# Optimization experiments

Hardware: AMD Instinct MI355X
Metric: run time of the kernel (lower is better)

Reference implementation:

```python
import jax, jax.numpy as jnp
import numpy as np

B, CQ, CM, K, O = 8, 128, 128, 128, 128
LQ, LK = 2048, 2048


def setup_inputs() -> dict:
    key = jax.random.key(0)
    ks = jax.random.split(key, 8)
    s = 0.05
    return {
        "x1": jax.random.normal(ks[0], (B, CQ, LQ), dtype=jnp.float32),
        "x2": jax.random.normal(ks[1], (B, CM, LK), dtype=jnp.float32),
        "Wq": jax.random.normal(ks[2], (K, CQ), dtype=jnp.float32) * s,
        "bq": jax.random.normal(ks[3], (K,), dtype=jnp.float32) * s,
        "Wk": jax.random.normal(ks[4], (K, CM), dtype=jnp.float32) * s,
        "bk": jax.random.normal(ks[5], (K,), dtype=jnp.float32) * s,
        "Wv": jax.random.normal(ks[6], (O, CM), dtype=jnp.float32) * s,
        "bv": jax.random.normal(ks[7], (O,), dtype=jnp.float32) * s,
    }


def reference(x1, x2, Wq, bq, Wk, bk, Wv, bv):
    # Conv1d with kernel_size=1 == per-position linear over channels
    q = jnp.einsum("bcq,kc->bkq", x1, Wq) + bq[None, :, None]  # (B,K,Lq)
    k = jnp.einsum("bcm,kc->bkm", x2, Wk) + bk[None, :, None]  # (B,K,Lk)
    v = jnp.einsum("bcm,oc->bom", x2, Wv) + bv[None, :, None]  # (B,O,Lk)
    # u[b,m,q] = sum_k q[b,k,q]*k[b,k,m] / sqrt(K)   -> (B,Lk,Lq)
    scale = 1.0 / np.sqrt(q.shape[1]).astype(np.float32)
    u = jnp.einsum("bkq,bkm->bmq", q, k) * scale
    w = jax.nn.softmax(u, axis=1)  # softmax over Lk (torch dim=1)
    # out[b,o,q] = sum_m w[b,m,q]*v[b,o,m]   -> (B,O,Lq)
    out = jnp.einsum("bmq,bom->boq", w, v)
    return (out, w)
```

## Files before the change

kernel.cpp:

```cpp
#include <hip/hip_runtime.h>
#include <cstddef>

#define B_ 8
#define C_ 128
#define K_ 128
#define L_ 2048

static constexpr float SCALE = 0.08838834764831843f;

typedef unsigned short u16;
typedef __attribute__((ext_vector_type(8))) short bf16x8;
typedef __attribute__((ext_vector_type(4))) unsigned short u16x4;
typedef __attribute__((ext_vector_type(4))) unsigned int u32x4;
typedef __attribute__((ext_vector_type(4))) float f32x4;
typedef __attribute__((ext_vector_type(16))) float f32x16;

__device__ __forceinline__ u16 f2bf(float x) {
    unsigned u = __builtin_bit_cast(unsigned, x);
    u += 0x7FFFu + ((u >> 16) & 1u);
    return (u16)(u >> 16);
}

__device__ __forceinline__ unsigned cvtpk(float lo, float hi) {
    unsigned r;
    asm("v_cvt_pk_bf16_f32 %0, %1, %2" : "=v"(r) : "v"(lo), "v"(hi));
    return r;
}
__device__ __forceinline__ void plswap(unsigned& a, unsigned& b) {
    asm volatile("v_permlane32_swap_b32 %0, %1" : "+v"(a), "+v"(b));
}

#define MFMA32 __builtin_amdgcn_mfma_f32_32x32x16_bf16


__global__ __launch_bounds__(256) void xpose_kernel(
    const float* __restrict__ x1, const float* __restrict__ x2,
    u16* __restrict__ xT1, u16* __restrict__ xT2)
{
    const int src = blockIdx.z;
    const int b   = blockIdx.y;
    const int l   = blockIdx.x * 128 + (threadIdx.x & 127);
    const int half = threadIdx.x >> 7;
    const float* X = src ? x2 : x1;
    u16* dst       = src ? xT2 : xT1;
    const float* xb = X + ((size_t)b * C_ + half * 64) * L_ + l;
    u16* db = dst + ((size_t)b * L_ + l) * C_ + half * 64;
    for (int c0 = 0; c0 < 64; c0 += 8) {
        bf16x8 pk;
        #pragma unroll
        for (int j = 0; j < 8; ++j)
            pk[j] = (short)f2bf(xb[(size_t)(c0 + j) * L_]);
        *(bf16x8*)(db + c0) = pk;
    }
}

__global__ __launch_bounds__(256) void proj_kernel(
    const u16* __restrict__ xT1, const u16* __restrict__ xT2,
    const float* __restrict__ Wq, const float* __restrict__ bq,
    const float* __restrict__ Wk, const float* __restrict__ bk,
    const float* __restrict__ Wv, const float* __restrict__ bv,
    u16* __restrict__ qF, u16* __restrict__ kF, u16* __restrict__ vF)
{
    const int l0 = blockIdx.x * 64;
    const int p  = blockIdx.y % 3;
    const int b  = blockIdx.y / 3;
    const float* W    = (p == 0) ? Wq : (p == 1) ? Wk : Wv;
    const float* bias = (p == 0) ? bq : (p == 1) ? bk : bv;
    const u16* xT     = (p == 0) ? xT1 : xT2;

    __shared__ u16 Wls[128 * 136];
    const int tid = threadIdx.x;
    for (int i = tid; i < 4096; i += 256) {
        float4 v = ((const float4*)W)[i];
        int e = i << 2; int row = e >> 7; int colc = e & 127;
        u16x4 pk = { f2bf(v.x), f2bf(v.y), f2bf(v.z), f2bf(v.w) };
        *(u16x4*)&Wls[row * 136 + colc] = pk;
    }
    __syncthreads();

    const int w = tid >> 6, l = tid & 63;
    const int lr = l & 15, lg = l >> 4;
    const int lrow = l0 + w * 16 + lr;

    bf16x8 xfr[4];
    const u16* xb = xT + ((size_t)b * L_ + lrow) * C_;
    #pragma unroll
    for (int s = 0; s < 4; ++s)
        xfr[s] = *(const bf16x8*)(xb + s * 32 + lg * 8);

    const int hl2 = lg >> 1, j0 = (lg & 1) * 4;

    for (int kt = 0; kt < 8; ++kt) {
        bf16x8 wfr[4];
        #pragma unroll
        for (int s = 0; s < 4; ++s)
            wfr[s] = *(const bf16x8*)&Wls[(kt * 16 + lr) * 136 + s * 32 + lg * 8];
        f32x4 acc = {0.f, 0.f, 0.f, 0.f};
        if (p < 2) {
            #pragma unroll
            for (int s = 0; s < 4; ++s)
                acc = __builtin_amdgcn_mfma_f32_16x16x32_bf16(wfr[s], xfr[s], acc, 0, 0, 0);
            u16x4 pk;
            #pragma unroll
            for (int r = 0; r < 4; ++r)
                pk[r] = f2bf(acc[r] + bias[kt * 16 + lg * 4 + r]);
            const int qt = lrow >> 5, qloc = lrow & 31;
            u16* dstp = ((p == 0) ? qF : kF)
                + (((size_t)b * 64 + qt) * 8 + kt) * 512 + hl2 * 256 + qloc * 8 + j0;
            *(u16x4*)dstp = pk;
        } else {
            #pragma unroll
            for (int s = 0; s < 4; ++s)
                acc = __builtin_amdgcn_mfma_f32_16x16x32_bf16(xfr[s], wfr[s], acc, 0, 0, 0);
            const int o = kt * 16 + lr;
            const float bo = bias[o];
            u16x4 pk;
            #pragma unroll
            for (int r = 0; r < 4; ++r)
                pk[r] = f2bf(acc[r] + bo);
            const int mt  = (l0 >> 5) + ((w * 16 + lg * 4) >> 5);
            const int t   = w & 1;
            const int ob  = kt >> 1;
            const int oloc = (kt & 1) * 16 + lr;
            u16* dstp = vF + ((size_t)b * 64 + mt) * 4096
                + ob * 1024 + t * 512 + hl2 * 256 + oloc * 8 + j0;
            *(u16x4*)dstp = pk;
        }
    }
}

__global__ __launch_bounds__(256, 2) void fused_attn_kernel(
    const u16* __restrict__ qF, const u16* __restrict__ kF,
    const u16* __restrict__ vF, float* __restrict__ out,
    float* __restrict__ wout)
{
    __shared__ float red[4 * 128 * 32];

    const int bid = blockIdx.x;
    const int b   = bid & 7;
    const int qt  = bid >> 3;
    const int q0  = qt * 32;
    const int tid = threadIdx.x;
    const int w   = tid >> 6;
    const int l   = tid & 63;
    const int col = l & 31;
    const int hl  = l >> 5;
    const int mz  = w * 512;

    bf16x8 qf[8];
    {
        const u16* qp = qF + (((size_t)b * 64 + qt) * 8) * 512 + l * 8;
        #pragma unroll
        for (int ks = 0; ks < 8; ++ks)
            qf[ks] = *(const bf16x8*)(qp + ks * 512);
    }

    const u16* kbase = kF + (((size_t)b * 64 + (mz >> 5)) * 8) * 512 + l * 8;
    const u16* vbase = vF + ((size_t)b * 64 + (mz >> 5)) * 4096 + l * 8;

    bf16x8 kA[8], kB[8];
    auto LK = [&](bf16x8 (&d)[8], int it) {
        const u16* ka = kbase + (size_t)it * 4096;
        #pragma unroll
        for (int j = 0; j < 8; ++j)
            d[j] = *(const bf16x8*)(ka + j * 512);
    };

    float csum = 0.f;
    auto STEPA = [&](bf16x8 (&kf)[8], bf16x8 (&kn)[8], int itn) {
        f32x16 sa = {}, sb = {};
        sa = MFMA32(kf[0], qf[0], sa, 0, 0, 0); sb = MFMA32(kf[4], qf[4], sb, 0, 0, 0);
        sa = MFMA32(kf[1], qf[1], sa, 0, 0, 0); sb = MFMA32(kf[5], qf[5], sb, 0, 0, 0);
        sa = MFMA32(kf[2], qf[2], sa, 0, 0, 0); sb = MFMA32(kf[6], qf[6], sb, 0, 0, 0);
        sa = MFMA32(kf[3], qf[3], sa, 0, 0, 0); sb = MFMA32(kf[7], qf[7], sb, 0, 0, 0);
        LK(kn, itn);
        float e[16];
        #pragma unroll
        for (int r = 0; r < 16; ++r)
            e[r] = __expf((sa[r] + sb[r]) * SCALE);
        float c0 = (e[0] + e[1]) + (e[2] + e[3]);
        float c1 = (e[4] + e[5]) + (e[6] + e[7]);
        float c2 = (e[8] + e[9]) + (e[10] + e[11]);
        float c3 = (e[12] + e[13]) + (e[14] + e[15]);
        csum += (c0 + c1) + (c2 + c3);
    };

    LK(kA, 0);
    for (int i2 = 0; i2 < 8; ++i2) {
        STEPA(kA, kB, 2 * i2 + 1);
        STEPA(kB, kA, (2 * i2 + 2) & 15);
    }

    csum += __shfl_xor(csum, 32);
    if (hl == 0) red[w * 32 + col] = csum;
    __syncthreads();
    const float rs = 1.0f / (red[col] + red[32 + col] + red[64 + col] + red[96 + col]);
    __syncthreads();

    f32x16 pv0 = {}, pv1 = {}, pv2 = {}, pv3 = {};

    auto STEPB = [&](bf16x8 (&kf)[8], int it, bf16x8 (&kn)[8]) {
        const u16* va = vbase + (size_t)it * 4096;
        bf16x8 vf[8];
        #pragma unroll
        for (int j = 0; j < 8; ++j)
            vf[j] = *(const bf16x8*)(va + j * 512);

        f32x16 sa = {}, sb = {};
        sa = MFMA32(kf[0], qf[0], sa, 0, 0, 0); sb = MFMA32(kf[4], qf[4], sb, 0, 0, 0);
        sa = MFMA32(kf[1], qf[1], sa, 0, 0, 0); sb = MFMA32(kf[5], qf[5], sb, 0, 0, 0);
        sa = MFMA32(kf[2], qf[2], sa, 0, 0, 0); sb = MFMA32(kf[6], qf[6], sb, 0, 0, 0);
        sa = MFMA32(kf[3], qf[3], sa, 0, 0, 0); sb = MFMA32(kf[7], qf[7], sb, 0, 0, 0);

        LK(kn, (it + 1) & 15);

        float e[16];
        #pragma unroll
        for (int r = 0; r < 16; ++r)
            e[r] = __expf((sa[r] + sb[r]) * SCALE);

        unsigned R0 = cvtpk(e[0], e[1]),   R1 = cvtpk(e[2], e[3]);
        unsigned R2 = cvtpk(e[4], e[5]),   R3 = cvtpk(e[6], e[7]);
        unsigned R4 = cvtpk(e[8], e[9]),   R5 = cvtpk(e[10], e[11]);
        unsigned R6 = cvtpk(e[12], e[13]), R7 = cvtpk(e[14], e[15]);
        plswap(R0, R2); plswap(R1, R3); plswap(R4, R6); plswap(R5, R7);
        u32x4 w0v = { R0, R1, R2, R3 };
        u32x4 w1v = { R4, R5, R6, R7 };
        bf16x8 B0 = __builtin_bit_cast(bf16x8, w0v);
        bf16x8 B1 = __builtin_bit_cast(bf16x8, w1v);

        pv0 = MFMA32(vf[0], B0, pv0, 0, 0, 0); pv1 = MFMA32(vf[2], B0, pv1, 0, 0, 0);
        pv2 = MFMA32(vf[4], B0, pv2, 0, 0, 0); pv3 = MFMA32(vf[6], B0, pv3, 0, 0, 0);
        pv0 = MFMA32(vf[1], B1, pv0, 0, 0, 0); pv1 = MFMA32(vf[3], B1, pv1, 0, 0, 0);
        pv2 = MFMA32(vf[5], B1, pv2, 0, 0, 0); pv3 = MFMA32(vf[7], B1, pv3, 0, 0, 0);

        float* wp = wout + ((size_t)b * L_ + mz + it * 32) * L_ + q0 + col;
        #pragma unroll
        for (int g = 0; g < 4; ++g)
            #pragma unroll
            for (int rr = 0; rr < 4; ++rr)
                wp[(size_t)(rr + 8 * g + 4 * hl) * L_] = e[4 * g + rr] * rs;
    };

    for (int i2 = 0; i2 < 8; ++i2) {
        STEPB(kA, 2 * i2,     kB);
        STEPB(kB, 2 * i2 + 1, kA);
    }

    {
        float* rp = red + (size_t)w * 128 * 32 + col;
        #pragma unroll
        for (int g = 0; g < 4; ++g)
            #pragma unroll
            for (int rr = 0; rr < 4; ++rr) {
                const int ol = rr + 8 * g + 4 * hl;
                rp[(ol)      * 32] = pv0[4 * g + rr];
                rp[(ol + 32) * 32] = pv1[4 * g + rr];
                rp[(ol + 64) * 32] = pv2[4 * g + rr];
                rp[(ol + 96) * 32] = pv3[4 * g + rr];
            }
    }
    __syncthreads();

    {
        const int qq = tid & 31;
        const int og = tid >> 5;
        float* ob = out + ((size_t)b * K_) * L_ + q0 + qq;
        #pragma unroll
        for (int i = 0; i < 16; ++i) {
            const int o = og + 8 * i;
            const float v = red[(0 * 128 + o) * 32 + qq] + red[(1 * 128 + o) * 32 + qq]
                          + red[(2 * 128 + o) * 32 + qq] + red[(3 * 128 + o) * 32 + qq];
            ob[(size_t)o * L_] = v * rs;
        }
    }
}

extern "C" void kernel_launch(void* const* d_in, const int* in_sizes, int n_in,
                              void* d_out, int out_size, void* d_ws, size_t ws_size,
                              hipStream_t stream) {
    (void)in_sizes; (void)n_in; (void)out_size; (void)ws_size;
    const float* x1 = (const float*)d_in[0];
    const float* x2 = (const float*)d_in[1];
    const float* Wq = (const float*)d_in[2];
    const float* bq = (const float*)d_in[3];
    const float* Wk = (const float*)d_in[4];
    const float* bk = (const float*)d_in[5];
    const float* Wv = (const float*)d_in[6];
    const float* bv = (const float*)d_in[7];

    float* out  = (float*)d_out;
    float* wout = out + (size_t)B_ * K_ * L_;

    const size_t NPROJ = (size_t)B_ * L_ * K_;
    u16* qF  = (u16*)d_ws;
    u16* kF  = qF  + NPROJ;
    u16* vF  = kF  + NPROJ;
    u16* xT1 = vF  + NPROJ;
    u16* xT2 = xT1 + NPROJ;

    xpose_kernel<<<dim3(L_ / 128, B_, 2), 256, 0, stream>>>(x1, x2, xT1, xT2);

    proj_kernel<<<dim3(L_ / 64, B_ * 3), 256, 0, stream>>>(
        xT1, xT2, Wq, bq, Wk, bk, Wv, bv, qF, kF, vF);

    fused_attn_kernel<<<dim3(512), 256, 0, stream>>>(qF, kF, vF, out, wout);
}
```

Baseline: 69.46 us.

## Split key range across 8 waves and cache exp scores in registers

Doubles the block to 512 threads so each wave covers 256 keys instead of 512, and stores the packed bf16 exponentials from the first pass in registers. This removes the recomputation of QK^T and exp in the second pass, which now only streams V and writes the normalized weights. The weights written out are now rounded from the bf16 values rather than taken from fp32, and the PV partials are reduced across the eight waves in two shared-memory stages. Register pressure rises from holding the cached scores and the double-buffered V fragments, which may limit occupancy.

```diff
diff --git a/kernel.cpp b/kernel.cpp
--- a/kernel.cpp
+++ b/kernel.cpp
@@ -129,12 +129,13 @@
     }
 }
 
-__global__ __launch_bounds__(256, 2) void fused_attn_kernel(
+__global__ __launch_bounds__(512, 2) void fused_attn_kernel(
     const u16* __restrict__ qF, const u16* __restrict__ kF,
     const u16* __restrict__ vF, float* __restrict__ out,
     float* __restrict__ wout)
 {
     __shared__ float red[4 * 128 * 32];
+    __shared__ float cred[8 * 32];
 
     const int bid = blockIdx.x;
     const int b   = bid & 7;
@@ -145,7 +146,6 @@
     const int l   = tid & 63;
     const int col = l & 31;
     const int hl  = l >> 5;
-    const int mz  = w * 512;
 
     bf16x8 qf[8];
     {
@@ -155,8 +155,11 @@
             qf[ks] = *(const bf16x8*)(qp + ks * 512);
     }
 
-    const u16* kbase = kF + (((size_t)b * 64 + (mz >> 5)) * 8) * 512 + l * 8;
-    const u16* vbase = vF + ((size_t)b * 64 + (mz >> 5)) * 4096 + l * 8;
+    const u16* kbase = kF + (((size_t)b * 64 + w * 8) * 8) * 512 + l * 8;
+    const u16* vbase = vF + ((size_t)b * 64 + w * 8) * 4096 + l * 8;
+
+    u32x4 ePA[8], ePB[8];
+    float csum = 0.f;
 
     bf16x8 kA[8], kB[8];
     auto LK = [&](bf16x8 (&d)[8], int it) {
@@ -166,14 +169,18 @@
             d[j] = *(const bf16x8*)(ka + j * 512);
     };
 
-    float csum = 0.f;
-    auto STEPA = [&](bf16x8 (&kf)[8], bf16x8 (&kn)[8], int itn) {
+    LK(kA, 0);
+    #pragma unroll
+    for (int it = 0; it < 8; ++it) {
+        bf16x8* kf = (it & 1) ? kB : kA;
+        bf16x8 (&kn)[8] = (it & 1) ? kA : kB;
         f32x16 sa = {}, sb = {};
         sa = MFMA32(kf[0], qf[0], sa, 0, 0, 0); sb = MFMA32(kf[4], qf[4], sb, 0, 0, 0);
         sa = MFMA32(kf[1], qf[1], sa, 0, 0, 0); sb = MFMA32(kf[5], qf[5], sb, 0, 0, 0);
         sa = MFMA32(kf[2], qf[2], sa, 0, 0, 0); sb = MFMA32(kf[6], qf[6], sb, 0, 0, 0);
         sa = MFMA32(kf[3], qf[3], sa, 0, 0, 0); sb = MFMA32(kf[7], qf[7], sb, 0, 0, 0);
-        LK(kn, itn);
+        if (it < 7) LK(kn, it + 1);
+
         float e[16];
         #pragma unroll
         for (int r = 0; r < 16; ++r)
@@ -183,72 +190,66 @@
         float c2 = (e[8] + e[9]) + (e[10] + e[11]);
         float c3 = (e[12] + e[13]) + (e[14] + e[15]);
         csum += (c0 + c1) + (c2 + c3);
-    };
-
-    LK(kA, 0);
-    for (int i2 = 0; i2 < 8; ++i2) {
-        STEPA(kA, kB, 2 * i2 + 1);
-        STEPA(kB, kA, (2 * i2 + 2) & 15);
-    }
-
-    csum += __shfl_xor(csum, 32);
-    if (hl == 0) red[w * 32 + col] = csum;
-    __syncthreads();
-    const float rs = 1.0f / (red[col] + red[32 + col] + red[64 + col] + red[96 + col]);
-    __syncthreads();
-
-    f32x16 pv0 = {}, pv1 = {}, pv2 = {}, pv3 = {};
-
-    auto STEPB = [&](bf16x8 (&kf)[8], int it, bf16x8 (&kn)[8]) {
-        const u16* va = vbase + (size_t)it * 4096;
-        bf16x8 vf[8];
-        #pragma unroll
-        for (int j = 0; j < 8; ++j)
-            vf[j] = *(const bf16x8*)(va + j * 512);
-
-        f32x16 sa = {}, sb = {};
-        sa = MFMA32(kf[0], qf[0], sa, 0, 0, 0); sb = MFMA32(kf[4], qf[4], sb, 0, 0, 0);
-        sa = MFMA32(kf[1], qf[1], sa, 0, 0, 0); sb = MFMA32(kf[5], qf[5], sb, 0, 0, 0);
-        sa = MFMA32(kf[2], qf[2], sa, 0, 0, 0); sb = MFMA32(kf[6], qf[6], sb, 0, 0, 0);
-        sa = MFMA32(kf[3], qf[3], sa, 0, 0, 0); sb = MFMA32(kf[7], qf[7], sb, 0, 0, 0);
-
-        LK(kn, (it + 1) & 15);
-
-        float e[16];
-        #pragma unroll
-        for (int r = 0; r < 16; ++r)
-            e[r] = __expf((sa[r] + sb[r]) * SCALE);
 
         unsigned R0 = cvtpk(e[0], e[1]),   R1 = cvtpk(e[2], e[3]);
         unsigned R2 = cvtpk(e[4], e[5]),   R3 = cvtpk(e[6], e[7]);
         unsigned R4 = cvtpk(e[8], e[9]),   R5 = cvtpk(e[10], e[11]);
         unsigned R6 = cvtpk(e[12], e[13]), R7 = cvtpk(e[14], e[15]);
         plswap(R0, R2); plswap(R1, R3); plswap(R4, R6); plswap(R5, R7);
-        u32x4 w0v = { R0, R1, R2, R3 };
-        u32x4 w1v = { R4, R5, R6, R7 };
-        bf16x8 B0 = __builtin_bit_cast(bf16x8, w0v);
-        bf16x8 B1 = __builtin_bit_cast(bf16x8, w1v);
+        ePA[it] = u32x4{ R0, R1, R2, R3 };
+        ePB[it] = u32x4{ R4, R5, R6, R7 };
+    }
+
+    csum += __shfl_xor(csum, 32);
+    if (hl == 0) cred[w * 32 + col] = csum;
+    __syncthreads();
+    const float rs = 1.0f / (((cred[col]       + cred[32 + col])
+                            + (cred[64 + col]  + cred[96 + col]))
+                           + ((cred[128 + col] + cred[160 + col])
+                            + (cred[192 + col] + cred[224 + col])));
+
+    f32x16 pv0 = {}, pv1 = {}, pv2 = {}, pv3 = {};
+
+    bf16x8 vA[8], vB[8];
+    auto LV = [&](bf16x8 (&d)[8], int it) {
+        const u16* va = vbase + (size_t)it * 4096;
+        #pragma unroll
+        for (int j = 0; j < 8; ++j)
+            d[j] = *(const bf16x8*)(va + j * 512);
+    };
+
+    LV(vA, 0);
+    #pragma unroll
+    for (int it = 0; it < 8; ++it) {
+        bf16x8* vf = (it & 1) ? vB : vA;
+        bf16x8 (&vn)[8] = (it & 1) ? vA : vB;
+        if (it < 7) LV(vn, it + 1);
+
+        bf16x8 B0 = __builtin_bit_cast(bf16x8, ePA[it]);
+        bf16x8 B1 = __builtin_bit_cast(bf16x8, ePB[it]);
 
         pv0 = MFMA32(vf[0], B0, pv0, 0, 0, 0); pv1 = MFMA32(vf[2], B0, pv1, 0, 0, 0);
         pv2 = MFMA32(vf[4], B0, pv2, 0, 0, 0); pv3 = MFMA32(vf[6], B0, pv3, 0, 0, 0);
         pv0 = MFMA32(vf[1], B1, pv0, 0, 0, 0); pv1 = MFMA32(vf[3], B1, pv1, 0, 0, 0);
         pv2 = MFMA32(vf[5], B1, pv2, 0, 0, 0); pv3 = MFMA32(vf[7], B1, pv3, 0, 0, 0);
 
-        float* wp = wout + ((size_t)b * L_ + mz + it * 32) * L_ + q0 + col;
-        #pragma unroll
-        for (int g = 0; g < 4; ++g)
-            #pragma unroll
-            for (int rr = 0; rr < 4; ++rr)
-                wp[(size_t)(rr + 8 * g + 4 * hl) * L_] = e[4 * g + rr] * rs;
-    };
-
-    for (int i2 = 0; i2 < 8; ++i2) {
-        STEPB(kA, 2 * i2,     kB);
-        STEPB(kB, 2 * i2 + 1, kA);
-    }
-
-    {
-        float* rp = red + (size_t)w * 128 * 32 + col;
+        float* wp = wout + ((size_t)b * L_ + w * 256 + it * 32 + hl * 8) * L_ + q0 + col;
+        #pragma unroll
+        for (int d = 0; d < 4; ++d) {
+            const unsigned da = ePA[it][d], db = ePB[it][d];
+            wp[(size_t)(2 * d) * L_]
+                = __builtin_bit_cast(float, da << 16) * rs;
+            wp[(size_t)(2 * d + 1) * L_]
+                = __builtin_bit_cast(float, da & 0xFFFF0000u) * rs;
+            wp[(size_t)(16 + 2 * d) * L_]
+                = __builtin_bit_cast(float, db << 16) * rs;
+            wp[(size_t)(16 + 2 * d + 1) * L_]
+                = __builtin_bit_cast(float, db & 0xFFFF0000u) * rs;
+        }
+    }
+
+    if (w >= 4) {
+        float* rp = red + (size_t)(w - 4) * 128 * 32 + col;
         #pragma unroll
         for (int g = 0; g < 4; ++g)
             #pragma unroll
@@ -261,14 +262,28 @@
             }
     }
     __syncthreads();
+    if (w < 4) {
+        float* rp = red + (size_t)w * 128 * 32 + col;
+        #pragma unroll
+        for (int g = 0; g < 4; ++g)
+            #pragma unroll
+            for (int rr = 0; rr < 4; ++rr) {
+                const int ol = rr + 8 * g + 4 * hl;
+                rp[(ol)      * 32] += pv0[4 * g + rr];
+                rp[(ol + 32) * 32] += pv1[4 * g + rr];
+                rp[(ol + 64) * 32] += pv2[4 * g + rr];
+                rp[(ol + 96) * 32] += pv3[4 * g + rr];
+            }
+    }
+    __syncthreads();
 
     {
         const int qq = tid & 31;
         const int og = tid >> 5;
         float* ob = out + ((size_t)b * K_) * L_ + q0 + qq;
         #pragma unroll
-        for (int i = 0; i < 16; ++i) {
-            const int o = og + 8 * i;
+        for (int i = 0; i < 8; ++i) {
+            const int o = og + 16 * i;
             const float v = red[(0 * 128 + o) * 32 + qq] + red[(1 * 128 + o) * 32 + qq]
                           + red[(2 * 128 + o) * 32 + qq] + red[(3 * 128 + o) * 32 + qq];
             ob[(size_t)o * L_] = v * rs;
@@ -304,5 +319,5 @@
     proj_kernel<<<dim3(L_ / 64, B_ * 3), 256, 0, stream>>>(
         xT1, xT2, Wq, bq, Wk, bk, Wv, bv, qF, kF, vF);
 
-    fused_attn_kernel<<<dim3(512), 256, 0, stream>>>(qF, kF, vF, out, wout);
-}
+    fused_attn_kernel<<<dim3(512), 512, 0, stream>>>(qF, kF, vF, out, wout);
+}
```

After: 65.57 us. 1.06x faster.

## Split fused attention into row-sum kernel and weight/PV kernel

Applied to the files above, without the earlier changes.

Splits the two-pass fused attention kernel into two launches. The first computes softmax denominators into a workspace buffer, and the second recomputes the scores, writes the normalized weights and accumulates P·V. This removes a block-wide barrier and the in-kernel phase switch, and fully unrolls the loops so the compiler can schedule them better. The cost is an extra kernel launch, a small global round-trip for the reciprocal sums, and re-reading q/k in a second kernel.

```diff
diff --git a/kernel.cpp b/kernel.cpp
--- a/kernel.cpp
+++ b/kernel.cpp
@@ -129,10 +129,76 @@
     }
 }
 
-__global__ __launch_bounds__(256, 2) void fused_attn_kernel(
+__global__ __launch_bounds__(256, 2) void rs_kernel(
     const u16* __restrict__ qF, const u16* __restrict__ kF,
-    const u16* __restrict__ vF, float* __restrict__ out,
-    float* __restrict__ wout)
+    float* __restrict__ rsb)
+{
+    __shared__ float cred[4 * 32];
+
+    const int bid = blockIdx.x;
+    const int b   = bid & 7;
+    const int qt  = bid >> 3;
+    const int tid = threadIdx.x;
+    const int w   = tid >> 6;
+    const int l   = tid & 63;
+    const int col = l & 31;
+    const int hl  = l >> 5;
+
+    bf16x8 qf[8];
+    {
+        const u16* qp = qF + (((size_t)b * 64 + qt) * 8) * 512 + l * 8;
+        #pragma unroll
+        for (int ks = 0; ks < 8; ++ks)
+            qf[ks] = *(const bf16x8*)(qp + ks * 512);
+    }
+
+    const u16* kbase = kF + (((size_t)b * 64 + w * 16) * 8) * 512 + l * 8;
+
+    bf16x8 kA[8], kB[8];
+    auto LK = [&](bf16x8 (&d)[8], int it) {
+        const u16* ka = kbase + (size_t)it * 4096;
+        #pragma unroll
+        for (int j = 0; j < 8; ++j)
+            d[j] = *(const bf16x8*)(ka + j * 512);
+    };
+
+    float csum = 0.f;
+    LK(kA, 0);
+    #pragma unroll
+    for (int it = 0; it < 16; ++it) {
+        bf16x8* kf = (it & 1) ? kB : kA;
+        bf16x8 (&kn)[8] = (it & 1) ? kA : kB;
+        f32x16 sa = {}, sb = {};
+        sa = MFMA32(kf[0], qf[0], sa, 0, 0, 0); sb = MFMA32(kf[4], qf[4], sb, 0, 0, 0);
+        sa = MFMA32(kf[1], qf[1], sa, 0, 0, 0); sb = MFMA32(kf[5], qf[5], sb, 0, 0, 0);
+        sa = MFMA32(kf[2], qf[2], sa, 0, 0, 0); sb = MFMA32(kf[6], qf[6], sb, 0, 0, 0);
+        sa = MFMA32(kf[3], qf[3], sa, 0, 0, 0); sb = MFMA32(kf[7], qf[7], sb, 0, 0, 0);
+        if (it < 15) LK(kn, it + 1);
+
+        float e[16];
+        #pragma unroll
+        for (int r = 0; r < 16; ++r)
+            e[r] = __expf((sa[r] + sb[r]) * SCALE);
+        float c0 = (e[0] + e[1]) + (e[2] + e[3]);
+        float c1 = (e[4] + e[5]) + (e[6] + e[7]);
+        float c2 = (e[8] + e[9]) + (e[10] + e[11]);
+        float c3 = (e[12] + e[13]) + (e[14] + e[15]);
+        csum += (c0 + c1) + (c2 + c3);
+    }
+
+    csum += __shfl_xor(csum, 32);
+    if (hl == 0) cred[w * 32 + col] = csum;
+    __syncthreads();
+    if (tid < 32) {
+        const float s = (cred[tid] + cred[32 + tid]) + (cred[64 + tid] + cred[96 + tid]);
+        rsb[(size_t)b * L_ + qt * 32 + tid] = 1.0f / s;
+    }
+}
+
+__global__ __launch_bounds__(256, 2) void wpv_kernel(
+    const u16* __restrict__ qF, const u16* __restrict__ kF,
+    const u16* __restrict__ vF, const float* __restrict__ rsb,
+    float* __restrict__ out, float* __restrict__ wout)
 {
     __shared__ float red[4 * 128 * 32];
 
@@ -154,9 +220,10 @@
         for (int ks = 0; ks < 8; ++ks)
             qf[ks] = *(const bf16x8*)(qp + ks * 512);
     }
-
-    const u16* kbase = kF + (((size_t)b * 64 + (mz >> 5)) * 8) * 512 + l * 8;
-    const u16* vbase = vF + ((size_t)b * 64 + (mz >> 5)) * 4096 + l * 8;
+    const float rs = rsb[(size_t)b * L_ + q0 + col];
+
+    const u16* kbase = kF + (((size_t)b * 64 + w * 16) * 8) * 512 + l * 8;
+    const u16* vbase = vF + ((size_t)b * 64 + w * 16) * 4096 + l * 8;
 
     bf16x8 kA[8], kB[8];
     auto LK = [&](bf16x8 (&d)[8], int it) {
@@ -166,58 +233,39 @@
             d[j] = *(const bf16x8*)(ka + j * 512);
     };
 
-    float csum = 0.f;
-    auto STEPA = [&](bf16x8 (&kf)[8], bf16x8 (&kn)[8], int itn) {
+    f32x16 pv0 = {}, pv1 = {}, pv2 = {}, pv3 = {};
+
+    LK(kA, 0);
+    #pragma unroll
+    for (int it = 0; it < 16; ++it) {
+        bf16x8* kf = (it & 1) ? kB : kA;
+        bf16x8 (&kn)[8] = (it & 1) ? kA : kB;
+
+        const u16* va = vbase + (size_t)it * 4096;
+        bf16x8 vf[8];
+        #pragma unroll
+        for (int j = 0; j < 8; ++j)
+            vf[j] = *(const bf16x8*)(va + j * 512);
+
         f32x16 sa = {}, sb = {};
         sa = MFMA32(kf[0], qf[0], sa, 0, 0, 0); sb = MFMA32(kf[4], qf[4], sb, 0, 0, 0);
         sa = MFMA32(kf[1], qf[1], sa, 0, 0, 0); sb = MFMA32(kf[5], qf[5], sb, 0, 0, 0);
         sa = MFMA32(kf[2], qf[2], sa, 0, 0, 0); sb = MFMA32(kf[6], qf[6], sb, 0, 0, 0);
         sa = MFMA32(kf[3], qf[3], sa, 0, 0, 0); sb = MFMA32(kf[7], qf[7], sb, 0, 0, 0);
-        LK(kn, itn);
+
+        if (it < 15) LK(kn, it + 1);
+
         float e[16];
         #pragma unroll
         for (int r = 0; r < 16; ++r)
             e[r] = __expf((sa[r] + sb[r]) * SCALE);
-        float c0 = (e[0] + e[1]) + (e[2] + e[3]);
-        float c1 = (e[4] + e[5]) + (e[6] + e[7]);
-        float c2 = (e[8] + e[9]) + (e[10] + e[11]);
-        float c3 = (e[12] + e[13]) + (e[14] + e[15]);
-        csum += (c0 + c1) + (c2 + c3);
-    };
-
-    LK(kA, 0);
-    for (int i2 = 0; i2 < 8; ++i2) {
-        STEPA(kA, kB, 2 * i2 + 1);
-        STEPA(kB, kA, (2 * i2 + 2) & 15);
-    }
-
-    csum += __shfl_xor(csum, 32);
-    if (hl == 0) red[w * 32 + col] = csum;
-    __syncthreads();
-    const float rs = 1.0f / (red[col] + red[32 + col] + red[64 + col] + red[96 + col]);
-    __syncthreads();
-
-    f32x16 pv0 = {}, pv1 = {}, pv2 = {}, pv3 = {};
-
-    auto STEPB = [&](bf16x8 (&kf)[8], int it, bf16x8 (&kn)[8]) {
-        const u16* va = vbase + (size_t)it * 4096;
-        bf16x8 vf[8];
-        #pragma unroll
-        for (int j = 0; j < 8; ++j)
-            vf[j] = *(const bf16x8*)(va + j * 512);
-
-        f32x16 sa = {}, sb = {};
-        sa = MFMA32(kf[0], qf[0], sa, 0, 0, 0); sb = MFMA32(kf[4], qf[4], sb, 0, 0, 0);
-        sa = MFMA32(kf[1], qf[1], sa, 0, 0, 0); sb = MFMA32(kf[5], qf[5], sb, 0, 0, 0);
-        sa = MFMA32(kf[2], qf[2], sa, 0, 0, 0); sb = MFMA32(kf[6], qf[6], sb, 0, 0, 0);
-        sa = MFMA32(kf[3], qf[3], sa, 0, 0, 0); sb = MFMA32(kf[7], qf[7], sb, 0, 0, 0);
-
-        LK(kn, (it + 1) & 15);
-
-        float e[16];
-        #pragma unroll
-        for (int r = 0; r < 16; ++r)
-            e[r] = __expf((sa[r] + sb[r]) * SCALE);
+
+        float* wp = wout + ((size_t)b * L_ + mz + it * 32) * L_ + q0 + col;
+        #pragma unroll
+        for (int g = 0; g < 4; ++g)
+            #pragma unroll
+            for (int rr = 0; rr < 4; ++rr)
+                wp[(size_t)(rr + 8 * g + 4 * hl) * L_] = e[4 * g + rr] * rs;
 
         unsigned R0 = cvtpk(e[0], e[1]),   R1 = cvtpk(e[2], e[3]);
         unsigned R2 = cvtpk(e[4], e[5]),   R3 = cvtpk(e[6], e[7]);
@@ -233,18 +281,6 @@
         pv2 = MFMA32(vf[4], B0, pv2, 0, 0, 0); pv3 = MFMA32(vf[6], B0, pv3, 0, 0, 0);
         pv0 = MFMA32(vf[1], B1, pv0, 0, 0, 0); pv1 = MFMA32(vf[3], B1, pv1, 0, 0, 0);
         pv2 = MFMA32(vf[5], B1, pv2, 0, 0, 0); pv3 = MFMA32(vf[7], B1, pv3, 0, 0, 0);
-
-        float* wp = wout + ((size_t)b * L_ + mz + it * 32) * L_ + q0 + col;
-        #pragma unroll
-        for (int g = 0; g < 4; ++g)
-            #pragma unroll
-            for (int rr = 0; rr < 4; ++rr)
-                wp[(size_t)(rr + 8 * g + 4 * hl) * L_] = e[4 * g + rr] * rs;
-    };
-
-    for (int i2 = 0; i2 < 8; ++i2) {
-        STEPB(kA, 2 * i2,     kB);
-        STEPB(kB, 2 * i2 + 1, kA);
     }
 
     {
@@ -298,11 +334,14 @@
     u16* vF  = kF  + NPROJ;
     u16* xT1 = vF  + NPROJ;
     u16* xT2 = xT1 + NPROJ;
+    float* rsb = (float*)(xT2 + NPROJ);
 
     xpose_kernel<<<dim3(L_ / 128, B_, 2), 256, 0, stream>>>(x1, x2, xT1, xT2);
 
     proj_kernel<<<dim3(L_ / 64, B_ * 3), 256, 0, stream>>>(
         xT1, xT2, Wq, bq, Wk, bk, Wv, bv, qF, kF, vF);
 
-    fused_attn_kernel<<<dim3(512), 256, 0, stream>>>(qF, kF, vF, out, wout);
-}
+    rs_kernel<<<dim3(512), 256, 0, stream>>>(qF, kF, rsb);
+
+    wpv_kernel<<<dim3(512), 256, 0, stream>>>(qF, kF, vF, rsb, out, wout);
+}
```

Result: slower. 72.62 us (+4.6%).
